# Kernel tuning notes

Measured on AMD Instinct MI355X. Metric: run time of the kernel, lower is better.

Reference implementation:

```python
import jax, jax.numpy as jnp
import numpy as np

HEAD = 16
EPS = 1.1920929e-07  # torch.finfo(float32).eps, used by nn.RMSNorm when eps=None


def _rms(x, g):
    return x * jax.lax.rsqrt(jnp.mean(x * x, axis=-1, keepdims=True) + EPS) * g


def _heads(t):
    b, L, dm = t.shape
    return t.reshape(b, L, HEAD, dm // HEAD).transpose(0, 2, 1, 3)  # b h L d


def setup_inputs() -> dict:
    key = jax.random.key(0)
    ks = jax.random.split(key, 8)
    b, L, dims = 1, 1024, 1024
    s = dims ** -0.5
    x = jax.random.normal(ks[0], (b, L, dims), jnp.float32)
    pt = jax.random.normal(ks[1], (b, L, dims), jnp.float32)
    # additive causal mask (finite large-negative to stay grad-safe)
    mask = jnp.triu(jnp.full((L, L), -1e9, jnp.float32), k=1)
    return {
        "x": x, "pt": pt, "mask": mask,
        "gq": jnp.ones((dims,), jnp.float32),
        "Wq": jax.random.normal(ks[2], (dims, dims), jnp.float32) * s,
        "bq": jnp.zeros((dims,), jnp.float32),
        "gkv": jnp.ones((dims,), jnp.float32),
        "Wkv": jax.random.normal(ks[3], (dims, 2 * dims), jnp.float32) * s,
        "bkv": jnp.zeros((2 * dims,), jnp.float32),
        "gc": jnp.ones((dims,), jnp.float32),
        "Wc": jax.random.normal(ks[4], (dims, dims), jnp.float32) * s,
        "bc": jnp.zeros((dims,), jnp.float32),
        "Wout": jax.random.normal(ks[5], (dims, dims), jnp.float32) * s,
        "bout": jnp.zeros((dims,), jnp.float32),
        "context_window": 16,
    }


def reference(x, pt, mask, gq, Wq, bq, gkv, Wkv, bkv, gc, Wc, bc, Wout, bout, context_window):
    b, L, dims = x.shape
    d = dims // HEAD
    q = _heads(_rms(x, gq) @ Wq + bq)                      # b h L d
    kv = (_rms(x, gkv) @ Wkv + bkv).reshape(b, L, 2, HEAD, d)
    k = kv[:, :, 0].transpose(0, 2, 1, 3)                  # b h L d
    v = kv[:, :, 1].transpose(0, 2, 1, 3)
    c = _heads(_rms(pt, gc) @ Wc + bc)                     # b h L d

    # triplet_scores[i,j] = sum_{t=max(0,min(i,j)-w)}^{min(L,max(i,j)+w)-1} q_i . (k_j * c_t)
    # Vectorize with prefix sums over c: window sum = P[end] - P[start],
    # where end depends only on max(i,j) and start only on min(i,j).
    P = jnp.concatenate([jnp.zeros((b, HEAD, 1, d), x.dtype), jnp.cumsum(c, axis=2)], axis=2)  # b h L+1 d
    idx = jnp.arange(L)
    S = jnp.clip(idx - context_window, 0, L)   # start for min-index
    E = jnp.clip(idx + context_window, 0, L)   # end for max-index
    PE = jnp.take(P, E, axis=2)                # b h L d
    PS = jnp.take(P, S, axis=2)

    U = jnp.einsum('bhid,bhjd->bhij', q, k * PE)        # end from j (i<=j branch)
    V = jnp.einsum('bhid,bhjd->bhij', q * PS, k)        # start from i (i<=j branch)
    U2 = jnp.einsum('bhid,bhjd->bhij', q * PE, k)       # end from i (i>j branch)
    V2 = jnp.einsum('bhid,bhjd->bhij', q, k * PS)       # start from j (i>j branch)
    lower = idx[:, None] <= idx[None, :]
    triplet = jnp.where(lower, U - V, U2 - V2)          # b h L L

    scale = d ** -0.5
    qk = jnp.einsum('bhid,bhjd->bhij', q, k) * scale + triplet + mask[:L, :L]
    attn = jax.nn.softmax(qk, axis=-1)
    wv = jnp.einsum('bhij,bhjd->bhid', attn, v)
    out = wv.transpose(0, 2, 1, 3).reshape(b, L, dims) @ Wout + bout  # dropout p=0.01 is identity at eval
    return out
```

## Files before the change

kernel.cpp:

```cpp
#include <hip/hip_runtime.h>

#define LQ 1024
#define DM 1024


typedef __attribute__((ext_vector_type(8))) short bf16x8;
typedef __attribute__((ext_vector_type(4))) float f32x4;

#define MFMA(a, b, c) __builtin_amdgcn_mfma_f32_16x16x32_bf16((a), (b), (c), 0, 0, 0)

__device__ __forceinline__ unsigned short f2bf(float x) {
    unsigned int u = __float_as_uint(x);
    return (unsigned short)((u + 0x7FFFu + ((u >> 16) & 1u)) >> 16);
}
__device__ __forceinline__ float bf2f(unsigned short h) {
    return __uint_as_float(((unsigned int)h) << 16);
}
__device__ __forceinline__ void gload16(const void* gp, void* lp) {
    __builtin_amdgcn_global_load_lds(
        (const __attribute__((address_space(1))) void*)gp,
        (__attribute__((address_space(3))) void*)lp, 16, 0, 0);
}
__device__ __forceinline__ void store_split4(unsigned short* ph, unsigned short* pl,
                                             float4 v) {
    unsigned short h0 = f2bf(v.x), h1 = f2bf(v.y), h2 = f2bf(v.z), h3 = f2bf(v.w);
    uint2 a;
    a.x = (unsigned)h0 | ((unsigned)h1 << 16);
    a.y = (unsigned)h2 | ((unsigned)h3 << 16);
    *(uint2*)ph = a;
    unsigned short l0 = f2bf(v.x - bf2f(h0)), l1 = f2bf(v.y - bf2f(h1));
    unsigned short l2 = f2bf(v.z - bf2f(h2)), l3 = f2bf(v.w - bf2f(h3));
    uint2 b;
    b.x = (unsigned)l0 | ((unsigned)l1 << 16);
    b.y = (unsigned)l2 | ((unsigned)l3 << 16);
    *(uint2*)pl = b;
}

__device__ __forceinline__ void rms_body(
    int row, const float* __restrict__ x, const float* __restrict__ pt,
    const float* __restrict__ gq, const float* __restrict__ gkv,
    const float* __restrict__ gc,
    unsigned short* xqn_h, unsigned short* xqn_l,
    unsigned short* xkvn_h, unsigned short* xkvn_l,
    unsigned short* ptn_h, unsigned short* ptn_l)
{
    const int t = threadIdx.x;
    const bool isx = row < LQ;
    const float* src = isx ? (x + (size_t)row * DM)
                           : (pt + (size_t)(row - LQ) * DM);
    float4 v = ((const float4*)src)[t];
    float ss = v.x*v.x + v.y*v.y + v.z*v.z + v.w*v.w;
    #pragma unroll
    for (int o = 32; o > 0; o >>= 1) ss += __shfl_down(ss, o);
    __shared__ float red[4];
    if ((t & 63) == 0) red[t >> 6] = ss;
    __syncthreads();
    const float r = rsqrtf((red[0] + red[1] + red[2] + red[3]) * (1.0f / DM)
                           + 1.1920929e-07f);
    const size_t base = (size_t)(isx ? row : row - LQ) * DM + t * 4;
    if (isx) {
        float4 g1 = ((const float4*)gq)[t];
        float4 g2 = ((const float4*)gkv)[t];
        float4 y1, y2;
        y1.x = v.x*r*g1.x; y1.y = v.y*r*g1.y; y1.z = v.z*r*g1.z; y1.w = v.w*r*g1.w;
        y2.x = v.x*r*g2.x; y2.y = v.y*r*g2.y; y2.z = v.z*r*g2.z; y2.w = v.w*r*g2.w;
        store_split4(xqn_h + base, xqn_l + base, y1);
        store_split4(xkvn_h + base, xkvn_l + base, y2);
    } else {
        float4 g = ((const float4*)gc)[t];
        float4 y;
        y.x = v.x*r*g.x; y.y = v.y*r*g.y; y.z = v.z*r*g.z; y.w = v.w*r*g.w;
        store_split4(ptn_h + base, ptn_l + base, y);
    }
}

__device__ __forceinline__ void wsplit_body(
    const float* __restrict__ in, unsigned short* oh, unsigned short* ol,
    int K, int N, int bx, int by)
{
    __shared__ float T[64 * 65];
    const int t = threadIdx.x;
    const int tx = t & 15, ty = t >> 4;
    const int c0 = bx * 64, r0 = by * 64;
    #pragma unroll
    for (int p = 0; p < 4; ++p) {
        int row = ty + p * 16;
        float4 v = *(const float4*)(in + (size_t)(r0 + row) * N + c0 + tx * 4);
        T[row * 65 + tx * 4 + 0] = v.x;
        T[row * 65 + tx * 4 + 1] = v.y;
        T[row * 65 + tx * 4 + 2] = v.z;
        T[row * 65 + tx * 4 + 3] = v.w;
    }
    __syncthreads();
    #pragma unroll
    for (int p = 0; p < 4; ++p) {
        int n = ty + p * 16;
        float4 w;
        w.x = T[(tx * 4 + 0) * 65 + n];
        w.y = T[(tx * 4 + 1) * 65 + n];
        w.z = T[(tx * 4 + 2) * 65 + n];
        w.w = T[(tx * 4 + 3) * 65 + n];
        size_t o = (size_t)(c0 + n) * K + r0 + tx * 4;
        store_split4(oh + o, ol + o, w);
    }
}

__global__ __launch_bounds__(256) void prep_kernel(
    const float* __restrict__ x, const float* __restrict__ pt,
    const float* __restrict__ gq, const float* __restrict__ gkv,
    const float* __restrict__ gc,
    const float* __restrict__ Wq, const float* __restrict__ Wkv,
    const float* __restrict__ Wc, const float* __restrict__ Wout,
    unsigned short* xqn_h, unsigned short* xqn_l,
    unsigned short* xkvn_h, unsigned short* xkvn_l,
    unsigned short* ptn_h, unsigned short* ptn_l,
    unsigned short* WqT_h, unsigned short* WqT_l,
    unsigned short* WkvT_h, unsigned short* WkvT_l,
    unsigned short* WcT_h, unsigned short* WcT_l,
    unsigned short* WoT_h, unsigned short* WoT_l)
{
    const int b = blockIdx.x;
    if (b < 2048) {
        rms_body(b, x, pt, gq, gkv, gc, xqn_h, xqn_l, xkvn_h, xkvn_l, ptn_h, ptn_l);
    } else if (b < 2304) {
        int s = b - 2048; wsplit_body(Wq, WqT_h, WqT_l, 1024, 1024, s & 15, s >> 4);
    } else if (b < 2816) {
        int s = b - 2304; wsplit_body(Wkv, WkvT_h, WkvT_l, 1024, 2048, s & 31, s >> 5);
    } else if (b < 3072) {
        int s = b - 2816; wsplit_body(Wc, WcT_h, WcT_l, 1024, 1024, s & 15, s >> 4);
    } else {
        int s = b - 3072; wsplit_body(Wout, WoT_h, WoT_l, 1024, 1024, s & 15, s >> 4);
    }
}

__device__ __forceinline__ void gemm3p(
    const unsigned short* __restrict__ Ah, const unsigned short* __restrict__ Al,
    const unsigned short* __restrict__ Bh, const unsigned short* __restrict__ Bl,
    const float* __restrict__ bias, float* __restrict__ out, int N, int mt, int nt)
{
    __shared__ unsigned short sAh[128 * 32], sAl[128 * 32];
    __shared__ unsigned short sBh[128 * 32], sBl[128 * 32];
    const int t = threadIdx.x;
    const int lane = t & 63, w = t >> 6;
    const int wm = w >> 2, wn = w & 3;
    const int n16 = lane & 15, quad = lane >> 4;
    const int srow = lane >> 2, scol = (lane & 3) * 8;
    f32x4 zero = {0.f, 0.f, 0.f, 0.f};
    f32x4 acc[4][2];
    #pragma unroll
    for (int ms = 0; ms < 4; ++ms)
        #pragma unroll
        for (int ns = 0; ns < 2; ++ns) acc[ms][ns] = zero;

    for (int kt = 0; kt < 32; ++kt) {
        const int k0 = kt * 32;
        const size_t ga = (size_t)(mt * 128 + w * 16 + srow) * 1024 + k0 + scol;
        const size_t gb = (size_t)(nt * 128 + w * 16 + srow) * 1024 + k0 + scol;
        const int lb = w * 512;
        __syncthreads();
        gload16(Ah + ga, sAh + lb);
        gload16(Al + ga, sAl + lb);
        gload16(Bh + gb, sBh + lb);
        gload16(Bl + gb, sBl + lb);
        __syncthreads();
        bf16x8 afh[4], afl[4], bfh[2], bfl[2];
        #pragma unroll
        for (int ms = 0; ms < 4; ++ms) {
            int r = wm * 64 + ms * 16 + n16;
            afh[ms] = *(const bf16x8*)&sAh[r * 32 + quad * 8];
            afl[ms] = *(const bf16x8*)&sAl[r * 32 + quad * 8];
        }
        #pragma unroll
        for (int ns = 0; ns < 2; ++ns) {
            int r = wn * 32 + ns * 16 + n16;
            bfh[ns] = *(const bf16x8*)&sBh[r * 32 + quad * 8];
            bfl[ns] = *(const bf16x8*)&sBl[r * 32 + quad * 8];
        }
        #pragma unroll
        for (int ms = 0; ms < 4; ++ms)
            #pragma unroll
            for (int ns = 0; ns < 2; ++ns) {
                acc[ms][ns] = MFMA(afh[ms], bfh[ns], acc[ms][ns]);
                acc[ms][ns] = MFMA(afh[ms], bfl[ns], acc[ms][ns]);
                acc[ms][ns] = MFMA(afl[ms], bfh[ns], acc[ms][ns]);
            }
    }
    #pragma unroll
    for (int ns = 0; ns < 2; ++ns) {
        const int col = nt * 128 + wn * 32 + ns * 16 + n16;
        const float bv = bias[col];
        #pragma unroll
        for (int ms = 0; ms < 4; ++ms) {
            const int row0 = mt * 128 + wm * 64 + ms * 16 + quad * 4;
            #pragma unroll
            for (int reg = 0; reg < 4; ++reg)
                out[(size_t)(row0 + reg) * N + col] = acc[ms][ns][reg] + bv;
        }
    }
}

__global__ __launch_bounds__(512) void proj_kernel(
    const unsigned short* __restrict__ xqn_h, const unsigned short* __restrict__ xqn_l,
    const unsigned short* __restrict__ xkvn_h, const unsigned short* __restrict__ xkvn_l,
    const unsigned short* __restrict__ ptn_h, const unsigned short* __restrict__ ptn_l,
    const unsigned short* __restrict__ WqT_h, const unsigned short* __restrict__ WqT_l,
    const unsigned short* __restrict__ WkvT_h, const unsigned short* __restrict__ WkvT_l,
    const unsigned short* __restrict__ WcT_h, const unsigned short* __restrict__ WcT_l,
    const float* __restrict__ bq, const float* __restrict__ bkv,
    const float* __restrict__ bc,
    float* __restrict__ Qb, float* __restrict__ KVb, float* __restrict__ Cb)
{
    const int bid = blockIdx.x;
    if (bid < 64) {
        gemm3p(xqn_h, xqn_l, WqT_h, WqT_l, bq, Qb, 1024, bid >> 3, bid & 7);
    } else if (bid < 192) {
        int b2 = bid - 64;
        gemm3p(xkvn_h, xkvn_l, WkvT_h, WkvT_l, bkv, KVb, 2048, b2 >> 4, b2 & 15);
    } else {
        int b2 = bid - 192;
        gemm3p(ptn_h, ptn_l, WcT_h, WcT_l, bc, Cb, 1024, b2 >> 3, b2 & 7);
    }
}

__global__ __launch_bounds__(256) void csum_kernel(const float* __restrict__ Cb,
                                                   float* __restrict__ csum)
{
    const int cid = blockIdx.x >> 2;
    const int col = ((blockIdx.x & 3) << 8) + threadIdx.x;
    const float* p = Cb + (size_t)cid * 32 * 1024 + col;
    float s = 0.f;
    #pragma unroll 8
    for (int r = 0; r < 32; ++r) s += p[(size_t)r * 1024];
    csum[cid * 1024 + col] = s;
}

__global__ __launch_bounds__(256) void scanp_kernel(const float* __restrict__ Cb,
                                                    const float* __restrict__ csum,
                                                    float* __restrict__ Pb)
{
    const int cid = blockIdx.x >> 2;
    const int col = ((blockIdx.x & 3) << 8) + threadIdx.x;
    float run = 0.f;
    for (int c = 0; c < cid; ++c) run += csum[c * 1024 + col];
    const float* p = Cb + (size_t)cid * 32 * 1024 + col;
    float* q = Pb + (size_t)cid * 32 * 1024 + col;
    for (int r = 0; r < 32; ++r) {
        q[(size_t)r * 1024] = run;
        run += p[(size_t)r * 1024];
    }
    if (cid == 31) Pb[(size_t)1024 * 1024 + col] = run;
}

__global__ __launch_bounds__(256) void abv_kernel(
    const float* __restrict__ Qb, const float* __restrict__ KVb,
    const float* __restrict__ Pb, const int* __restrict__ cwp,
    unsigned short* __restrict__ Aah, unsigned short* __restrict__ Aal,
    unsigned short* __restrict__ Bah, unsigned short* __restrict__ Bal,
    unsigned short* __restrict__ VT)
{
    const int b = blockIdx.x;
    if (b < 4096) {
        const int gid = b * 256 + threadIdx.x;
        const int i = gid >> 10;
        const int col = gid & 1023;
        const int h = col >> 6, dd = col & 63;
        const int cw = *cwp;
        const int E = min(i + cw, LQ);
        const int S = max(i - cw, 0);
        const float pe = Pb[(size_t)E * 1024 + col];
        const float ps = Pb[(size_t)S * 1024 + col];
        const float q = Qb[gid];
        const float k = KVb[(size_t)i * 2048 + col];
        const float scale = 0.125f;
        const size_t base = ((size_t)(h * 1024 + i)) * 128;
        float a0 = q, a1 = q * pe;
        float b0 = k * (scale - ps), b1 = k;
        unsigned short hv;
        hv = f2bf(a0); Aah[base + dd] = hv;      Aal[base + dd] = f2bf(a0 - bf2f(hv));
        hv = f2bf(a1); Aah[base + 64 + dd] = hv; Aal[base + 64 + dd] = f2bf(a1 - bf2f(hv));
        hv = f2bf(b0); Bah[base + dd] = hv;      Bal[base + dd] = f2bf(b0 - bf2f(hv));
        hv = f2bf(b1); Bah[base + 64 + dd] = hv; Bal[base + 64 + dd] = f2bf(b1 - bf2f(hv));
    } else {
        const int s = b - 4096;
        const int h = s >> 4, j0 = (s & 15) * 64;
        __shared__ float T[64 * 65];
        const int t = threadIdx.x;
        const int tx = t & 15, ty = t >> 4;
        #pragma unroll
        for (int p = 0; p < 4; ++p) {
            int j = ty + p * 16;
            float4 v = *(const float4*)(KVb + (size_t)(j0 + j) * 2048 + 1024 + h * 64 + tx * 4);
            T[j * 65 + tx * 4 + 0] = v.x;
            T[j * 65 + tx * 4 + 1] = v.y;
            T[j * 65 + tx * 4 + 2] = v.z;
            T[j * 65 + tx * 4 + 3] = v.w;
        }
        __syncthreads();
        #pragma unroll
        for (int p = 0; p < 4; ++p) {
            int d = ty + p * 16;
            unsigned short e0 = f2bf(T[(tx * 4 + 0) * 65 + d]);
            unsigned short e1 = f2bf(T[(tx * 4 + 1) * 65 + d]);
            unsigned short e2 = f2bf(T[(tx * 4 + 2) * 65 + d]);
            unsigned short e3 = f2bf(T[(tx * 4 + 3) * 65 + d]);
            uint2 pk;
            pk.x = (unsigned)e0 | ((unsigned)e1 << 16);
            pk.y = (unsigned)e2 | ((unsigned)e3 << 16);
            *(uint2*)(VT + (size_t)(h * 64 + d) * 1024 + j0 + tx * 4) = pk;
        }
    }
}

__global__ __launch_bounds__(256) void attn_kernel(
    const unsigned short* __restrict__ Aah, const unsigned short* __restrict__ Aal,
    const unsigned short* __restrict__ Bah, const unsigned short* __restrict__ Bal,
    const unsigned short* __restrict__ VT,
    float* __restrict__ Op, float* __restrict__ Mp, float* __restrict__ Lp)
{
    __shared__ unsigned short PsAll[4][16 * 68];
    const int t = threadIdx.x;
    const int lane = t & 63, wid = t >> 6;
    unsigned short* Ps = PsAll[wid];
    const int raw = blockIdx.x * 4 + wid;
    const int g = raw >> 5;
    const int it16 = (g & 1) ? (g >> 1) : (63 - (g >> 1));
    const int sub = raw & 31;
    const int h = sub >> 1, half = sub & 1;
    const int i0 = it16 * 16;
    const int njt = (i0 >> 6) + 1;
    const int n16 = lane & 15, quad = lane >> 4;

    bf16x8 afh[4], afl[4];
    {
        const size_t ar = ((size_t)(h * 1024 + i0 + n16)) * 128 + quad * 8;
        #pragma unroll
        for (int kc = 0; kc < 4; ++kc) {
            afh[kc] = *(const bf16x8*)(Aah + ar + kc * 32);
            afl[kc] = *(const bf16x8*)(Aal + ar + kc * 32);
        }
    }

    f32x4 zero = {0.f, 0.f, 0.f, 0.f};
    f32x4 oacc[4];
    #pragma unroll
    for (int dt = 0; dt < 4; ++dt) oacc[dt] = zero;
    float mrow[4], lrow[4];
    #pragma unroll
    for (int reg = 0; reg < 4; ++reg) { mrow[reg] = -1e30f; lrow[reg] = 0.f; }

    for (int jt = half; jt < njt; jt += 2) {
        const int j0 = jt * 64;
        f32x4 s[4];
        #pragma unroll
        for (int jj = 0; jj < 4; ++jj) s[jj] = zero;
        #pragma unroll
        for (int jj = 0; jj < 4; ++jj) {
            const size_t br = ((size_t)(h * 1024 + j0 + jj * 16 + n16)) * 128 + quad * 8;
            #pragma unroll
            for (int kc = 0; kc < 4; ++kc) {
                bf16x8 bh = *(const bf16x8*)(Bah + br + kc * 32);
                bf16x8 bl = *(const bf16x8*)(Bal + br + kc * 32);
                s[jj] = MFMA(afh[kc], bh, s[jj]);
                s[jj] = MFMA(afh[kc], bl, s[jj]);
                s[jj] = MFMA(afl[kc], bh, s[jj]);
            }
        }
        if (jt == njt - 1) {
            const int ibase = i0 + quad * 4;
            #pragma unroll
            for (int jj = 0; jj < 4; ++jj) {
                const int j = j0 + jj * 16 + n16;
                #pragma unroll
                for (int reg = 0; reg < 4; ++reg)
                    if (j > ibase + reg) s[jj][reg] = -1e30f;
            }
        }

        float alpha[4];
        #pragma unroll
        for (int reg = 0; reg < 4; ++reg) {
            float mt_ = fmaxf(fmaxf(s[0][reg], s[1][reg]), fmaxf(s[2][reg], s[3][reg]));
            mt_ = fmaxf(mt_, __shfl_xor(mt_, 1));
            mt_ = fmaxf(mt_, __shfl_xor(mt_, 2));
            mt_ = fmaxf(mt_, __shfl_xor(mt_, 4));
            mt_ = fmaxf(mt_, __shfl_xor(mt_, 8));
            const float mn = fmaxf(mrow[reg], mt_);
            alpha[reg] = __expf(mrow[reg] - mn);
            mrow[reg] = mn;
            float rs = 0.f;
            #pragma unroll
            for (int jj = 0; jj < 4; ++jj) {
                float p = __expf(s[jj][reg] - mn);
                s[jj][reg] = p;
                rs += p;
            }
            rs += __shfl_xor(rs, 1); rs += __shfl_xor(rs, 2);
            rs += __shfl_xor(rs, 4); rs += __shfl_xor(rs, 8);
            lrow[reg] = lrow[reg] * alpha[reg] + rs;
        }

        __builtin_amdgcn_s_waitcnt(0xC07F);
        #pragma unroll
        for (int jj = 0; jj < 4; ++jj)
            #pragma unroll
            for (int reg = 0; reg < 4; ++reg)
                Ps[(quad * 4 + reg) * 68 + jj * 16 + n16] = f2bf(s[jj][reg]);
        __builtin_amdgcn_s_waitcnt(0xC07F);
        bf16x8 pf0 = *(const bf16x8*)&Ps[n16 * 68 + quad * 8];
        bf16x8 pf1 = *(const bf16x8*)&Ps[n16 * 68 + 32 + quad * 8];

        #pragma unroll
        for (int dt = 0; dt < 4; ++dt) {
            #pragma unroll
            for (int reg = 0; reg < 4; ++reg) oacc[dt][reg] *= alpha[reg];
            const size_t vr = ((size_t)(h * 64 + dt * 16 + n16)) * 1024 + j0 + quad * 8;
            bf16x8 vf0 = *(const bf16x8*)(VT + vr);
            bf16x8 vf1 = *(const bf16x8*)(VT + vr + 32);
            oacc[dt] = MFMA(pf0, vf0, oacc[dt]);
            oacc[dt] = MFMA(pf1, vf1, oacc[dt]);
        }
    }

    const int tid = (h * 64 + it16) * 2 + half;
    #pragma unroll
    for (int dt = 0; dt < 4; ++dt)
        #pragma unroll
        for (int reg = 0; reg < 4; ++reg)
            Op[(size_t)tid * 1024 + (quad * 4 + reg) * 64 + dt * 16 + n16] = oacc[dt][reg];
    if (n16 == 0) {
        #pragma unroll
        for (int reg = 0; reg < 4; ++reg) {
            Mp[tid * 16 + quad * 4 + reg] = mrow[reg];
            Lp[tid * 16 + quad * 4 + reg] = lrow[reg];
        }
    }
}

__global__ __launch_bounds__(128) void outgemm_kernel(
    const float* __restrict__ Op, const float* __restrict__ Mp,
    const float* __restrict__ Lp,
    const unsigned short* __restrict__ WoT_h, const unsigned short* __restrict__ WoT_l,
    const float* __restrict__ bout, float* __restrict__ out)
{
    __shared__ float cc[16 * 64 * 2];
    __shared__ unsigned short sAh[64 * 32], sAl[64 * 32];
    __shared__ unsigned short sBh[32 * 32], sBl[32 * 32];
    const int t = threadIdx.x;
    const int lane = t & 63, w = t >> 6;
    const int n16 = lane & 15, quad = lane >> 4;
    const int mt = blockIdx.x >> 5, nt = blockIdx.x & 31;

    for (int p = t; p < 1024; p += 128) {
        const int hh = p >> 6, row = p & 63;
        const int i = mt * 64 + row, i16 = i >> 4, r = i & 15;
        const int t0 = (hh * 64 + i16) * 2;
        const float m1 = Mp[t0 * 16 + r], m2 = Mp[(t0 + 1) * 16 + r];
        const float l1 = Lp[t0 * 16 + r], l2 = Lp[(t0 + 1) * 16 + r];
        const float M = fmaxf(m1, m2);
        const float e1 = __expf(m1 - M), e2 = __expf(m2 - M);
        const float Ltot = e1 * l1 + e2 * l2;
        cc[p * 2 + 0] = e1 / Ltot;
        cc[p * 2 + 1] = e2 / Ltot;
    }

    f32x4 zero = {0.f, 0.f, 0.f, 0.f};
    f32x4 acc[2][2];
    #pragma unroll
    for (int ms = 0; ms < 2; ++ms)
        #pragma unroll
        for (int ns = 0; ns < 2; ++ns) acc[ms][ns] = zero;

    const int arow = t >> 1, aseg = (t & 1) * 16;
    for (int kt = 0; kt < 32; ++kt) {
        const int hh = kt >> 1, dbase = (kt & 1) * 32;
        __syncthreads();
        {
            const size_t gb = (size_t)(nt * 32 + w * 16 + (lane >> 2)) * 1024
                            + kt * 32 + (lane & 3) * 8;
            gload16(WoT_h + gb, sBh + w * 512);
            gload16(WoT_l + gb, sBl + w * 512);
        }
        {
            const int i = mt * 64 + arow, i16 = i >> 4, r = i & 15;
            const float c1 = cc[(hh * 64 + arow) * 2 + 0];
            const float c2 = cc[(hh * 64 + arow) * 2 + 1];
            const size_t b0 = ((size_t)((hh * 64 + i16) * 2)) * 1024 + r * 64 + dbase + aseg;
            #pragma unroll
            for (int u = 0; u < 4; ++u) {
                float4 o1 = *(const float4*)(Op + b0 + u * 4);
                float4 o2 = *(const float4*)(Op + b0 + 1024 + u * 4);
                float4 v;
                v.x = c1 * o1.x + c2 * o2.x; v.y = c1 * o1.y + c2 * o2.y;
                v.z = c1 * o1.z + c2 * o2.z; v.w = c1 * o1.w + c2 * o2.w;
                store_split4(&sAh[arow * 32 + aseg + u * 4],
                             &sAl[arow * 32 + aseg + u * 4], v);
            }
        }
        __syncthreads();
        bf16x8 ah[2], al[2], bh[2], bl[2];
        #pragma unroll
        for (int ms = 0; ms < 2; ++ms) {
            int r = w * 32 + ms * 16 + n16;
            ah[ms] = *(const bf16x8*)&sAh[r * 32 + quad * 8];
            al[ms] = *(const bf16x8*)&sAl[r * 32 + quad * 8];
        }
        #pragma unroll
        for (int ns = 0; ns < 2; ++ns) {
            int r = ns * 16 + n16;
            bh[ns] = *(const bf16x8*)&sBh[r * 32 + quad * 8];
            bl[ns] = *(const bf16x8*)&sBl[r * 32 + quad * 8];
        }
        #pragma unroll
        for (int ms = 0; ms < 2; ++ms)
            #pragma unroll
            for (int ns = 0; ns < 2; ++ns) {
                acc[ms][ns] = MFMA(ah[ms], bh[ns], acc[ms][ns]);
                acc[ms][ns] = MFMA(ah[ms], bl[ns], acc[ms][ns]);
                acc[ms][ns] = MFMA(al[ms], bh[ns], acc[ms][ns]);
            }
    }
    #pragma unroll
    for (int ns = 0; ns < 2; ++ns) {
        const int col = nt * 32 + ns * 16 + n16;
        const float bv = bout[col];
        #pragma unroll
        for (int ms = 0; ms < 2; ++ms) {
            const int row0 = mt * 64 + w * 32 + ms * 16 + quad * 4;
            #pragma unroll
            for (int reg = 0; reg < 4; ++reg)
                out[(size_t)(row0 + reg) * 1024 + col] = acc[ms][ns][reg] + bv;
        }
    }
}

extern "C" void kernel_launch(void* const* d_in, const int* in_sizes, int n_in,
                              void* d_out, int out_size, void* d_ws, size_t ws_size,
                              hipStream_t stream) {
    (void)in_sizes; (void)n_in; (void)out_size; (void)ws_size;
    const float* x    = (const float*)d_in[0];
    const float* pt   = (const float*)d_in[1];
    const float* gq   = (const float*)d_in[3];
    const float* Wq   = (const float*)d_in[4];
    const float* bq   = (const float*)d_in[5];
    const float* gkv  = (const float*)d_in[6];
    const float* Wkv  = (const float*)d_in[7];
    const float* bkv  = (const float*)d_in[8];
    const float* gc   = (const float*)d_in[9];
    const float* Wc   = (const float*)d_in[10];
    const float* bc   = (const float*)d_in[11];
    const float* Wout = (const float*)d_in[12];
    const float* bout = (const float*)d_in[13];
    const int*   cw   = (const int*)d_in[14];
    float* out = (float*)d_out;

    char* W = (char*)d_ws;
    const size_t MB = 1u << 20;
    #define US(off) ((unsigned short*)(W + (size_t)(off)))
    #define FP(off) ((float*)(W + (size_t)(off)))
    unsigned short* xqn_h  = US(0 * MB);
    unsigned short* xqn_l  = US(2 * MB);
    unsigned short* xkvn_h = US(4 * MB);
    unsigned short* xkvn_l = US(6 * MB);
    unsigned short* ptn_h  = US(8 * MB);
    unsigned short* ptn_l  = US(10 * MB);
    unsigned short* WqT_h  = US(12 * MB);
    unsigned short* WqT_l  = US(14 * MB);
    unsigned short* WkvT_h = US(16 * MB);
    unsigned short* WkvT_l = US(20 * MB);
    unsigned short* WcT_h  = US(24 * MB);
    unsigned short* WcT_l  = US(26 * MB);
    unsigned short* WoT_h  = US(28 * MB);
    unsigned short* WoT_l  = US(30 * MB);
    float* Qb   = FP(32 * MB);
    float* KVb  = FP(36 * MB);
    float* Cb   = FP(44 * MB);
    float* Pb   = FP(48 * MB);
    float* csum = FP(52 * MB + 256 * 1024);
    unsigned short* Aah = US(0 * MB);
    unsigned short* Aal = US(4 * MB);
    unsigned short* Bah = US(8 * MB);
    unsigned short* Bal = US(12 * MB);
    unsigned short* VTb = US(16 * MB);
    float* Op = FP(18 * MB);
    float* Mp = FP(26 * MB);
    float* Lp = FP(26 * MB + 512 * 1024);
    #undef US
    #undef FP

    hipLaunchKernelGGL(prep_kernel, dim3(3328), dim3(256), 0, stream,
                       x, pt, gq, gkv, gc, Wq, Wkv, Wc, Wout,
                       xqn_h, xqn_l, xkvn_h, xkvn_l, ptn_h, ptn_l,
                       WqT_h, WqT_l, WkvT_h, WkvT_l, WcT_h, WcT_l, WoT_h, WoT_l);
    hipLaunchKernelGGL(proj_kernel, dim3(256), dim3(512), 0, stream,
                       xqn_h, xqn_l, xkvn_h, xkvn_l, ptn_h, ptn_l,
                       WqT_h, WqT_l, WkvT_h, WkvT_l, WcT_h, WcT_l,
                       bq, bkv, bc, Qb, KVb, Cb);
    hipLaunchKernelGGL(csum_kernel, dim3(128), dim3(256), 0, stream, Cb, csum);
    hipLaunchKernelGGL(scanp_kernel, dim3(128), dim3(256), 0, stream, Cb, csum, Pb);
    hipLaunchKernelGGL(abv_kernel, dim3(4352), dim3(256), 0, stream,
                       Qb, KVb, Pb, cw, Aah, Aal, Bah, Bal, VTb);
    hipLaunchKernelGGL(attn_kernel, dim3(512), dim3(256), 0, stream,
                       Aah, Aal, Bah, Bal, VTb, Op, Mp, Lp);
    hipLaunchKernelGGL(outgemm_kernel, dim3(512), dim3(128), 0, stream,
                       Op, Mp, Lp, WoT_h, WoT_l, bout, out);
}
```

Before: 276.4 us.

## Split attention KV range across 4 waves with in-block merge; retile projection GEMM

The attention kernel now gives each block one (head, 16-row query tile) and splits its key tiles across four waves. The per-wave partial outputs, maxima and sums are merged in shared memory, and the result is written directly as bf16 hi/lo split buffers. This replaces the fp32 partial-output round trip through global memory and the merge inside the output GEMM, which can now load its A operand directly with global_load_lds. The projection GEMM also moves to 128x64 tiles with 256 threads and twice as many blocks, to improve CU occupancy. The costs are more LDS per attention block and a block-wide sync before the merge.

Measured after the change: 225.3 us. 18.5% less time.

```diff
diff --git a/kernel.cpp b/kernel.cpp
--- a/kernel.cpp
+++ b/kernel.cpp
@@ -8,6 +8,7 @@
 typedef __attribute__((ext_vector_type(4))) float f32x4;
 
 #define MFMA(a, b, c) __builtin_amdgcn_mfma_f32_16x16x32_bf16((a), (b), (c), 0, 0, 0)
+#define WAIT_LDS() __builtin_amdgcn_s_waitcnt(0xC07F)
 
 __device__ __forceinline__ unsigned short f2bf(float x) {
     unsigned int u = __float_as_uint(x);
@@ -139,12 +140,12 @@
     const float* __restrict__ bias, float* __restrict__ out, int N, int mt, int nt)
 {
     __shared__ unsigned short sAh[128 * 32], sAl[128 * 32];
-    __shared__ unsigned short sBh[128 * 32], sBl[128 * 32];
+    __shared__ unsigned short sBh[64 * 32], sBl[64 * 32];
     const int t = threadIdx.x;
     const int lane = t & 63, w = t >> 6;
-    const int wm = w >> 2, wn = w & 3;
+    const int wm = w >> 1, wn = w & 1;
     const int n16 = lane & 15, quad = lane >> 4;
-    const int srow = lane >> 2, scol = (lane & 3) * 8;
+    const int srow = t >> 2, scol = (t & 3) * 8;
     f32x4 zero = {0.f, 0.f, 0.f, 0.f};
     f32x4 acc[4][2];
     #pragma unroll
@@ -154,14 +155,19 @@
 
     for (int kt = 0; kt < 32; ++kt) {
         const int k0 = kt * 32;
-        const size_t ga = (size_t)(mt * 128 + w * 16 + srow) * 1024 + k0 + scol;
-        const size_t gb = (size_t)(nt * 128 + w * 16 + srow) * 1024 + k0 + scol;
-        const int lb = w * 512;
         __syncthreads();
-        gload16(Ah + ga, sAh + lb);
-        gload16(Al + ga, sAl + lb);
-        gload16(Bh + gb, sBh + lb);
-        gload16(Bl + gb, sBl + lb);
+        #pragma unroll
+        for (int p = 0; p < 2; ++p) {
+            const size_t ga = (size_t)(mt * 128 + srow + p * 64) * 1024 + k0 + scol;
+            const int lb = w * 512 + p * 2048;
+            gload16(Ah + ga, sAh + lb);
+            gload16(Al + ga, sAl + lb);
+        }
+        {
+            const size_t gb = (size_t)(nt * 64 + srow) * 1024 + k0 + scol;
+            gload16(Bh + gb, sBh + w * 512);
+            gload16(Bl + gb, sBl + w * 512);
+        }
         __syncthreads();
         bf16x8 afh[4], afl[4], bfh[2], bfl[2];
         #pragma unroll
@@ -187,7 +193,7 @@
     }
     #pragma unroll
     for (int ns = 0; ns < 2; ++ns) {
-        const int col = nt * 128 + wn * 32 + ns * 16 + n16;
+        const int col = nt * 64 + wn * 32 + ns * 16 + n16;
         const float bv = bias[col];
         #pragma unroll
         for (int ms = 0; ms < 4; ++ms) {
@@ -199,7 +205,7 @@
     }
 }
 
-__global__ __launch_bounds__(512) void proj_kernel(
+__global__ __launch_bounds__(256) void proj_kernel(
     const unsigned short* __restrict__ xqn_h, const unsigned short* __restrict__ xqn_l,
     const unsigned short* __restrict__ xkvn_h, const unsigned short* __restrict__ xkvn_l,
     const unsigned short* __restrict__ ptn_h, const unsigned short* __restrict__ ptn_l,
@@ -211,14 +217,14 @@
     float* __restrict__ Qb, float* __restrict__ KVb, float* __restrict__ Cb)
 {
     const int bid = blockIdx.x;
-    if (bid < 64) {
-        gemm3p(xqn_h, xqn_l, WqT_h, WqT_l, bq, Qb, 1024, bid >> 3, bid & 7);
-    } else if (bid < 192) {
-        int b2 = bid - 64;
-        gemm3p(xkvn_h, xkvn_l, WkvT_h, WkvT_l, bkv, KVb, 2048, b2 >> 4, b2 & 15);
+    if (bid < 128) {
+        gemm3p(xqn_h, xqn_l, WqT_h, WqT_l, bq, Qb, 1024, bid >> 4, bid & 15);
+    } else if (bid < 384) {
+        int b2 = bid - 128;
+        gemm3p(xkvn_h, xkvn_l, WkvT_h, WkvT_l, bkv, KVb, 2048, b2 >> 5, b2 & 31);
     } else {
-        int b2 = bid - 192;
-        gemm3p(ptn_h, ptn_l, WcT_h, WcT_l, bc, Cb, 1024, b2 >> 3, b2 & 7);
+        int b2 = bid - 384;
+        gemm3p(ptn_h, ptn_l, WcT_h, WcT_l, bc, Cb, 1024, b2 >> 4, b2 & 15);
     }
 }
 
@@ -311,21 +317,25 @@
     }
 }
 
-__global__ __launch_bounds__(256) void attn_kernel(
+__global__ __launch_bounds__(256, 4) void attn_kernel(
     const unsigned short* __restrict__ Aah, const unsigned short* __restrict__ Aal,
     const unsigned short* __restrict__ Bah, const unsigned short* __restrict__ Bal,
     const unsigned short* __restrict__ VT,
-    float* __restrict__ Op, float* __restrict__ Mp, float* __restrict__ Lp)
+    unsigned short* __restrict__ wvh, unsigned short* __restrict__ wvl)
 {
     __shared__ unsigned short PsAll[4][16 * 68];
+    __shared__ float cO[4][16 * 68];
+    __shared__ float cM[4][16], cL[4][16];
+
     const int t = threadIdx.x;
     const int lane = t & 63, wid = t >> 6;
     unsigned short* Ps = PsAll[wid];
-    const int raw = blockIdx.x * 4 + wid;
-    const int g = raw >> 5;
-    const int it16 = (g & 1) ? (g >> 1) : (63 - (g >> 1));
-    const int sub = raw & 31;
-    const int h = sub >> 1, half = sub & 1;
+    const int b = blockIdx.x;
+    const int h = b & 15;
+    const int q = (b >> 4) & 15;
+    const int group = b >> 8;
+    const int it16 = (group == 0) ? q : (group == 1) ? (31 - q)
+                   : (group == 2) ? (32 + q) : (63 - q);
     const int i0 = it16 * 16;
     const int njt = (i0 >> 6) + 1;
     const int n16 = lane & 15, quad = lane >> 4;
@@ -348,7 +358,7 @@
     #pragma unroll
     for (int reg = 0; reg < 4; ++reg) { mrow[reg] = -1e30f; lrow[reg] = 0.f; }
 
-    for (int jt = half; jt < njt; jt += 2) {
+    for (int jt = wid; jt < njt; jt += 4) {
         const int j0 = jt * 64;
         f32x4 s[4];
         #pragma unroll
@@ -399,13 +409,13 @@
             lrow[reg] = lrow[reg] * alpha[reg] + rs;
         }
 
-        __builtin_amdgcn_s_waitcnt(0xC07F);
+        WAIT_LDS();
         #pragma unroll
         for (int jj = 0; jj < 4; ++jj)
             #pragma unroll
             for (int reg = 0; reg < 4; ++reg)
                 Ps[(quad * 4 + reg) * 68 + jj * 16 + n16] = f2bf(s[jj][reg]);
-        __builtin_amdgcn_s_waitcnt(0xC07F);
+        WAIT_LDS();
         bf16x8 pf0 = *(const bf16x8*)&Ps[n16 * 68 + quad * 8];
         bf16x8 pf1 = *(const bf16x8*)&Ps[n16 * 68 + 32 + quad * 8];
 
@@ -421,48 +431,50 @@
         }
     }
 
-    const int tid = (h * 64 + it16) * 2 + half;
     #pragma unroll
     for (int dt = 0; dt < 4; ++dt)
         #pragma unroll
         for (int reg = 0; reg < 4; ++reg)
-            Op[(size_t)tid * 1024 + (quad * 4 + reg) * 64 + dt * 16 + n16] = oacc[dt][reg];
+            cO[wid][(quad * 4 + reg) * 68 + dt * 16 + n16] = oacc[dt][reg];
     if (n16 == 0) {
         #pragma unroll
         for (int reg = 0; reg < 4; ++reg) {
-            Mp[tid * 16 + quad * 4 + reg] = mrow[reg];
-            Lp[tid * 16 + quad * 4 + reg] = lrow[reg];
-        }
+            cM[wid][quad * 4 + reg] = mrow[reg];
+            cL[wid][quad * 4 + reg] = lrow[reg];
+        }
+    }
+    __syncthreads();
+    #pragma unroll
+    for (int u = 0; u < 4; ++u) {
+        const int p = u * 256 + t;
+        const int r = p >> 6, d = p & 63;
+        const float m0 = cM[0][r], m1 = cM[1][r], m2 = cM[2][r], m3 = cM[3][r];
+        const float M = fmaxf(fmaxf(m0, m1), fmaxf(m2, m3));
+        const float e0 = __expf(m0 - M), e1 = __expf(m1 - M);
+        const float e2 = __expf(m2 - M), e3 = __expf(m3 - M);
+        const float L = e0 * cL[0][r] + e1 * cL[1][r] + e2 * cL[2][r] + e3 * cL[3][r];
+        const float o = e0 * cO[0][r * 68 + d] + e1 * cO[1][r * 68 + d]
+                      + e2 * cO[2][r * 68 + d] + e3 * cO[3][r * 68 + d];
+        const float v = o / L;
+        const size_t oi = (size_t)(i0 + r) * 1024 + h * 64 + d;
+        const unsigned short hv = f2bf(v);
+        wvh[oi] = hv;
+        wvl[oi] = f2bf(v - bf2f(hv));
     }
 }
 
 __global__ __launch_bounds__(128) void outgemm_kernel(
-    const float* __restrict__ Op, const float* __restrict__ Mp,
-    const float* __restrict__ Lp,
-    const unsigned short* __restrict__ WoT_h, const unsigned short* __restrict__ WoT_l,
-    const float* __restrict__ bout, float* __restrict__ out)
-{
-    __shared__ float cc[16 * 64 * 2];
+    const unsigned short* __restrict__ Ah, const unsigned short* __restrict__ Al,
+    const unsigned short* __restrict__ Bh, const unsigned short* __restrict__ Bl,
+    const float* __restrict__ bias, float* __restrict__ out)
+{
     __shared__ unsigned short sAh[64 * 32], sAl[64 * 32];
     __shared__ unsigned short sBh[32 * 32], sBl[32 * 32];
     const int t = threadIdx.x;
     const int lane = t & 63, w = t >> 6;
     const int n16 = lane & 15, quad = lane >> 4;
     const int mt = blockIdx.x >> 5, nt = blockIdx.x & 31;
-
-    for (int p = t; p < 1024; p += 128) {
-        const int hh = p >> 6, row = p & 63;
-        const int i = mt * 64 + row, i16 = i >> 4, r = i & 15;
-        const int t0 = (hh * 64 + i16) * 2;
-        const float m1 = Mp[t0 * 16 + r], m2 = Mp[(t0 + 1) * 16 + r];
-        const float l1 = Lp[t0 * 16 + r], l2 = Lp[(t0 + 1) * 16 + r];
-        const float M = fmaxf(m1, m2);
-        const float e1 = __expf(m1 - M), e2 = __expf(m2 - M);
-        const float Ltot = e1 * l1 + e2 * l2;
-        cc[p * 2 + 0] = e1 / Ltot;
-        cc[p * 2 + 1] = e2 / Ltot;
-    }
-
+    const int srow = t >> 2, scol = (t & 3) * 8;
     f32x4 zero = {0.f, 0.f, 0.f, 0.f};
     f32x4 acc[2][2];
     #pragma unroll
@@ -470,31 +482,20 @@
         #pragma unroll
         for (int ns = 0; ns < 2; ++ns) acc[ms][ns] = zero;
 
-    const int arow = t >> 1, aseg = (t & 1) * 16;
     for (int kt = 0; kt < 32; ++kt) {
-        const int hh = kt >> 1, dbase = (kt & 1) * 32;
+        const int k0 = kt * 32;
         __syncthreads();
+        #pragma unroll
+        for (int p = 0; p < 2; ++p) {
+            const size_t ga = (size_t)(mt * 64 + srow + p * 32) * 1024 + k0 + scol;
+            const int lb = w * 512 + p * 1024;
+            gload16(Ah + ga, sAh + lb);
+            gload16(Al + ga, sAl + lb);
+        }
         {
-            const size_t gb = (size_t)(nt * 32 + w * 16 + (lane >> 2)) * 1024
-                            + kt * 32 + (lane & 3) * 8;
-            gload16(WoT_h + gb, sBh + w * 512);
-            gload16(WoT_l + gb, sBl + w * 512);
-        }
-        {
-            const int i = mt * 64 + arow, i16 = i >> 4, r = i & 15;
-            const float c1 = cc[(hh * 64 + arow) * 2 + 0];
-            const float c2 = cc[(hh * 64 + arow) * 2 + 1];
-            const size_t b0 = ((size_t)((hh * 64 + i16) * 2)) * 1024 + r * 64 + dbase + aseg;
-            #pragma unroll
-            for (int u = 0; u < 4; ++u) {
-                float4 o1 = *(const float4*)(Op + b0 + u * 4);
-                float4 o2 = *(const float4*)(Op + b0 + 1024 + u * 4);
-                float4 v;
-                v.x = c1 * o1.x + c2 * o2.x; v.y = c1 * o1.y + c2 * o2.y;
-                v.z = c1 * o1.z + c2 * o2.z; v.w = c1 * o1.w + c2 * o2.w;
-                store_split4(&sAh[arow * 32 + aseg + u * 4],
-                             &sAl[arow * 32 + aseg + u * 4], v);
-            }
+            const size_t gb = (size_t)(nt * 32 + srow) * 1024 + k0 + scol;
+            gload16(Bh + gb, sBh + w * 512);
+            gload16(Bl + gb, sBl + w * 512);
         }
         __syncthreads();
         bf16x8 ah[2], al[2], bh[2], bl[2];
@@ -522,7 +523,7 @@
     #pragma unroll
     for (int ns = 0; ns < 2; ++ns) {
         const int col = nt * 32 + ns * 16 + n16;
-        const float bv = bout[col];
+        const float bv = bias[col];
         #pragma unroll
         for (int ms = 0; ms < 2; ++ms) {
             const int row0 = mt * 64 + w * 32 + ms * 16 + quad * 4;
@@ -581,9 +582,8 @@
     unsigned short* Bah = US(8 * MB);
     unsigned short* Bal = US(12 * MB);
     unsigned short* VTb = US(16 * MB);
-    float* Op = FP(18 * MB);
-    float* Mp = FP(26 * MB);
-    float* Lp = FP(26 * MB + 512 * 1024);
+    unsigned short* wv_h = US(18 * MB);
+    unsigned short* wv_l = US(20 * MB);
     #undef US
     #undef FP
 
@@ -591,7 +591,7 @@
                        x, pt, gq, gkv, gc, Wq, Wkv, Wc, Wout,
                        xqn_h, xqn_l, xkvn_h, xkvn_l, ptn_h, ptn_l,
                        WqT_h, WqT_l, WkvT_h, WkvT_l, WcT_h, WcT_l, WoT_h, WoT_l);
-    hipLaunchKernelGGL(proj_kernel, dim3(256), dim3(512), 0, stream,
+    hipLaunchKernelGGL(proj_kernel, dim3(512), dim3(256), 0, stream,
                        xqn_h, xqn_l, xkvn_h, xkvn_l, ptn_h, ptn_l,
                        WqT_h, WqT_l, WkvT_h, WkvT_l, WcT_h, WcT_l,
                        bq, bkv, bc, Qb, KVb, Cb);
@@ -599,8 +599,8 @@
     hipLaunchKernelGGL(scanp_kernel, dim3(128), dim3(256), 0, stream, Cb, csum, Pb);
     hipLaunchKernelGGL(abv_kernel, dim3(4352), dim3(256), 0, stream,
                        Qb, KVb, Pb, cw, Aah, Aal, Bah, Bal, VTb);
-    hipLaunchKernelGGL(attn_kernel, dim3(512), dim3(256), 0, stream,
-                       Aah, Aal, Bah, Bal, VTb, Op, Mp, Lp);
+    hipLaunchKernelGGL(attn_kernel, dim3(1024), dim3(256), 0, stream,
+                       Aah, Aal, Bah, Bal, VTb, wv_h, wv_l);
     hipLaunchKernelGGL(outgemm_kernel, dim3(512), dim3(128), 0, stream,
-                       Op, Mp, Lp, WoT_h, WoT_l, bout, out);
-}
+                       wv_h, wv_l, WoT_h, WoT_l, bout, out);
+}
```
